# Optimization experiments

Measured on AMD Instinct MI355X. Metric: run time of the kernel, lower is better.

Reference implementation:

```python
import jax, jax.numpy as jnp
import numpy as np

B, T, D = 2, 2048, 1024
H, DH, P = 16, 64, 512


def setup_inputs() -> dict:
    key = jax.random.key(0)
    ks = jax.random.split(key, 7)
    s = 0.02
    return {
        "x": jax.random.normal(ks[0], (B, T, D), jnp.float32),
        "prefix_k": jax.random.normal(ks[1], (B, H, P, DH), jnp.float32),
        "prefix_v": jax.random.normal(ks[2], (B, H, P, DH), jnp.float32),
        "Wq": jax.random.normal(ks[3], (D, D), jnp.float32) * s,
        "Wk": jax.random.normal(ks[4], (D, D), jnp.float32) * s,
        "Wv": jax.random.normal(ks[5], (D, D), jnp.float32) * s,
        "Wo": jax.random.normal(ks[6], (D, D), jnp.float32) * s,
    }


def reference(x, prefix_k, prefix_v, Wq, Wk, Wv, Wo):
    b, t, c = x.shape
    h, dh = H, DH
    # nn.Linear without bias: y = x @ W.T
    q = (x @ Wq.T).reshape(b, t, h, dh).transpose(0, 2, 1, 3)  # [B,H,T,Dh]
    k = (x @ Wk.T).reshape(b, t, h, dh).transpose(0, 2, 1, 3)
    v = (x @ Wv.T).reshape(b, t, h, dh).transpose(0, 2, 1, 3)
    k = jnp.concatenate([prefix_k, k], axis=2)  # [B,H,P+T,Dh]
    v = jnp.concatenate([prefix_v, v], axis=2)
    scale = 1.0 / jnp.sqrt(jnp.float32(dh))
    att = jnp.einsum("bhqd,bhkd->bhqk", q, k) * scale  # [B,H,T,P+T]
    att = jax.nn.softmax(att, axis=-1)  # no causal mask in source
    y = jnp.einsum("bhqk,bhkd->bhqd", att, v)  # [B,H,T,Dh]
    y = y.transpose(0, 2, 1, 3).reshape(b, t, c)
    return y @ Wo.T
```

## Files before the change

### kernel.cpp

```cpp
#include <hip/hip_runtime.h>
#include <cstdint>

#define Bv  2
#define Tv  2048
#define Dv  1024
#define Hv  16
#define DHv 64
#define Pv  512
#define Lv  2560

typedef __attribute__((ext_vector_type(8))) short sh8;
typedef __attribute__((ext_vector_type(4))) short sh4;
typedef __attribute__((ext_vector_type(4))) float f4;
typedef __attribute__((ext_vector_type(4))) unsigned int u4v;

#define MFMA(a,b,c) __builtin_amdgcn_mfma_f32_16x16x32_bf16(a,b,c,0,0,0)

__device__ __forceinline__ unsigned short bf16_rn(float f) {
    unsigned int u = __builtin_bit_cast(unsigned int, f);
    u += 0x7FFFu + ((u >> 16) & 1u);
    return (unsigned short)(u >> 16);
}
__device__ __forceinline__ float bf16_f(unsigned short h) {
    unsigned int u = ((unsigned int)h) << 16;
    return __builtin_bit_cast(float, u);
}
__device__ __forceinline__ unsigned int fbits(float f) {
    return __builtin_bit_cast(unsigned int, f);
}

__device__ __forceinline__ void gload16(const unsigned short* g, unsigned short* l) {
    __builtin_amdgcn_global_load_lds(
        (const __attribute__((address_space(1))) unsigned int*)(g),
        (__attribute__((address_space(3))) unsigned int*)(l),
        16, 0, 0);
}

__device__ __forceinline__ sh8 packP(const f4 a, const f4 b) {
    float e0 = __builtin_amdgcn_exp2f(a[0]), e1 = __builtin_amdgcn_exp2f(a[1]);
    float e2 = __builtin_amdgcn_exp2f(a[2]), e3 = __builtin_amdgcn_exp2f(a[3]);
    float f0 = __builtin_amdgcn_exp2f(b[0]), f1 = __builtin_amdgcn_exp2f(b[1]);
    float f2 = __builtin_amdgcn_exp2f(b[2]), f3 = __builtin_amdgcn_exp2f(b[3]);
    u4v d;
    d[0] = __builtin_amdgcn_perm(fbits(e1), fbits(e0), 0x07060302u);
    d[1] = __builtin_amdgcn_perm(fbits(e3), fbits(e2), 0x07060302u);
    d[2] = __builtin_amdgcn_perm(fbits(f1), fbits(f0), 0x07060302u);
    d[3] = __builtin_amdgcn_perm(fbits(f3), fbits(f2), 0x07060302u);
    return __builtin_bit_cast(sh8, d);
}

__global__ __launch_bounds__(256) void prep_convert(
    const float* __restrict__ x,  const float* __restrict__ Wq,
    const float* __restrict__ Wk, const float* __restrict__ Wv,
    const float* __restrict__ pk, const float* __restrict__ Wo,
    unsigned short* __restrict__ xb,  unsigned short* __restrict__ wqb,
    unsigned short* __restrict__ wkb, unsigned short* __restrict__ wvb,
    unsigned short* __restrict__ pkb, unsigned short* __restrict__ woh)
{
    int i = blockIdx.x * 256 + threadIdx.x;
    const float* src; unsigned short* dst; int off;
    if      (i < 1048576) { src = x;  dst = xb;  off = i; }
    else if (i < 1310720) { src = Wq; dst = wqb; off = i - 1048576; }
    else if (i < 1572864) { src = Wk; dst = wkb; off = i - 1310720; }
    else if (i < 1835008) { src = Wv; dst = wvb; off = i - 1572864; }
    else if (i < 2097152) { src = pk; dst = pkb; off = i - 1835008; }
    else                  { src = Wo; dst = woh; off = i - 2097152; }
    float4 v = reinterpret_cast<const float4*>(src)[off];
    sh4 h;
    h[0] = (short)bf16_rn(v.x); h[1] = (short)bf16_rn(v.y);
    h[2] = (short)bf16_rn(v.z); h[3] = (short)bf16_rn(v.w);
    reinterpret_cast<sh4*>(dst)[off] = h;
}

__global__ __launch_bounds__(256) void prep_transpose(
    const float* __restrict__ pv, unsigned short* __restrict__ pvtb)
{
    __shared__ unsigned short Tls[64][66];
    const int tid = threadIdx.x;
    const int bh = blockIdx.x >> 3, pt = blockIdx.x & 7;
    #pragma unroll
    for (int i = 0; i < 4; i++) {
        int id = i * 256 + tid;
        int p = id >> 4, c4 = (id & 15) << 2;
        float4 v = *reinterpret_cast<const float4*>(
            &pv[((size_t)bh * Pv + pt * 64 + p) * DHv + c4]);
        Tls[c4+0][p] = bf16_rn(v.x);
        Tls[c4+1][p] = bf16_rn(v.y);
        Tls[c4+2][p] = bf16_rn(v.z);
        Tls[c4+3][p] = bf16_rn(v.w);
    }
    __syncthreads();
    #pragma unroll
    for (int i = 0; i < 2; i++) {
        int id = i * 256 + tid;
        int d = id >> 3, u = id & 7;
        sh4 lo, hi;
        #pragma unroll
        for (int j = 0; j < 4; j++) {
            lo[j] = (short)Tls[d][u * 8 + j];
            hi[j] = (short)Tls[d][u * 8 + 4 + j];
        }
        int p0 = ((u >> 2) & 1) * 32 + (u & 1) * 16 + ((u >> 1) & 1) * 4;
        size_t base = ((size_t)bh * DHv + d) * Pv + pt * 64;
        *reinterpret_cast<sh4*>(&pvtb[base + p0])     = lo;
        *reinterpret_cast<sh4*>(&pvtb[base + p0 + 8]) = hi;
    }
}

__global__ __launch_bounds__(256) void qkv_gemm(
    const unsigned short* __restrict__ xb,
    const unsigned short* __restrict__ wqb, const unsigned short* __restrict__ wkb,
    const unsigned short* __restrict__ wvb,
    unsigned short* __restrict__ qb, unsigned short* __restrict__ kb,
    unsigned short* __restrict__ vtb)
{
    __shared__ __align__(16) unsigned short As[128 * 64], Bs[128 * 64];
    const int tid = threadIdx.x;
    const int lane = tid & 63, w = tid >> 6;
    const int g = lane >> 4, tx = lane & 15;
    const int wr = w >> 1, wc = w & 1;
    const int m0 = blockIdx.x * 128, n0 = blockIdx.y * 128;
    const int z = blockIdx.z;
    const unsigned short* Wb = (z == 0) ? wqb : (z == 1) ? wkb : wvb;
    const int srow = lane >> 3, scol = lane & 7;

    f4 acc[4][4] = {};

    for (int k0 = 0; k0 < Dv; k0 += 64) {
        #pragma unroll
        for (int c = 0; c < 4; c++) {
            int row = w * 32 + c * 8 + srow;
            int su = (scol ^ (row & 7)) << 3;
            gload16(&xb[(size_t)(m0 + row) * Dv + k0 + su], &As[(w * 32 + c * 8) * 64]);
            gload16(&Wb[(size_t)(n0 + row) * Dv + k0 + su], &Bs[(w * 32 + c * 8) * 64]);
        }
        __syncthreads();
        #pragma unroll
        for (int ks = 0; ks < 2; ks++) {
            sh8 fa[4], fb[4];
            #pragma unroll
            for (int mi = 0; mi < 4; mi++) {
                int r = wr * 64 + mi * 16 + tx;
                fa[mi] = *reinterpret_cast<const sh8*>(&As[(r * 64 + ks * 32 + g * 8) ^ ((r & 7) << 3)]);
            }
            #pragma unroll
            for (int ni = 0; ni < 4; ni++) {
                int r = wc * 64 + ni * 16 + tx;
                fb[ni] = *reinterpret_cast<const sh8*>(&Bs[(r * 64 + ks * 32 + g * 8) ^ ((r & 7) << 3)]);
            }
            if (z < 2) {
                #pragma unroll
                for (int mi = 0; mi < 4; mi++)
                    #pragma unroll
                    for (int ni = 0; ni < 4; ni++)
                        acc[mi][ni] = MFMA(fb[ni], fa[mi], acc[mi][ni]);
            } else {
                #pragma unroll
                for (int mi = 0; mi < 4; mi++)
                    #pragma unroll
                    for (int ni = 0; ni < 4; ni++)
                        acc[mi][ni] = MFMA(fa[mi], fb[ni], acc[mi][ni]);
            }
        }
        __syncthreads();
    }

    if (z < 2) {
        unsigned short* ob = (z == 0) ? qb : kb;
        const float sc = (z == 0) ? 0.1803368801f : 1.0f;
        #pragma unroll
        for (int mi = 0; mi < 4; mi++)
            #pragma unroll
            for (int ni = 0; ni < 4; ni++) {
                int m = m0 + wr * 64 + mi * 16 + tx;
                int n = n0 + wc * 64 + ni * 16 + g * 4;
                sh4 pkd;
                #pragma unroll
                for (int i = 0; i < 4; i++) pkd[i] = (short)bf16_rn(acc[mi][ni][i] * sc);
                *reinterpret_cast<sh4*>(&ob[(size_t)m * Dv + n]) = pkd;
            }
    } else {
        const int tb0 = ((m0 + wr * 64) & (Tv - 1));
        const int b   = (m0 + wr * 64) >> 11;
        #pragma unroll
        for (int mi = 0; mi < 4; mi++)
            #pragma unroll
            for (int ni = 0; ni < 4; ni++) {
                int t = tb0 + ((mi & 2) << 4) + (g << 3) + ((mi & 1) << 2);
                int n = n0 + wc * 64 + ni * 16 + tx;
                int h = n >> 6, dh = n & 63;
                sh4 pkd;
                #pragma unroll
                for (int i = 0; i < 4; i++) pkd[i] = (short)bf16_rn(acc[mi][ni][i]);
                *reinterpret_cast<sh4*>(&vtb[(((size_t)(b * Hv + h)) * DHv + dh) * Tv + t]) = pkd;
            }
    }
}

__global__ __launch_bounds__(256) void flash_mfma(
    const unsigned short* __restrict__ qbuf, const unsigned short* __restrict__ kb,
    const unsigned short* __restrict__ vtb,
    const unsigned short* __restrict__ pkb, const unsigned short* __restrict__ pvtb,
    unsigned short* __restrict__ yh)
{
    __shared__ __align__(16) unsigned short Ks[2][64 * 64], Vs[2][64 * 64];
    __shared__ float olex[2][4][64];
    const int tid = threadIdx.x;
    const int lane = tid & 63, w = tid >> 6;
    const int kw = w & 1, qw = w >> 1;
    const int g = lane >> 4, tx = lane & 15;
    const int pblk = blockIdx.x;
    const int L = (pblk & 7) * 64 + (pblk >> 3);
    const int qt = L & 15;
    const int bh = L >> 4;
    const int b = bh >> 4, h = bh & 15;
    const int srow = lane >> 3, scol = lane & 7;

    sh8 qf[4][2];
    #pragma unroll
    for (int qg = 0; qg < 4; qg++) {
        size_t base = ((size_t)(b * Tv) + qt * 128 + qw * 64 + qg * 16 + tx) * Dv + h * 64;
        qf[qg][0] = *reinterpret_cast<const sh8*>(&qbuf[base + g * 8]);
        qf[qg][1] = *reinterpret_cast<const sh8*>(&qbuf[base + 32 + g * 8]);
    }

    f4 o[4][4] = {};
    f4 ol[4] = {};
    sh8 onesf;
    #pragma unroll
    for (int j = 0; j < 8; j++) onesf[j] = (short)0x3F80;

    const int r0 = w * 16 + srow, r1 = r0 + 8;
    const int su0 = (scol ^ (r0 & 7)) << 3;
    const int su1 = (scol ^ (r1 & 7)) << 3;
    const unsigned short* ka0 = &pkb[((size_t)bh * Pv + r0) * DHv + su0];
    const unsigned short* ka1 = &pkb[((size_t)bh * Pv + r1) * DHv + su1];
    const unsigned short* va0 = &pvtb[((size_t)bh * DHv + r0) * Pv + su0];
    const unsigned short* va1 = &pvtb[((size_t)bh * DHv + r1) * Pv + su1];

    auto stage = [&](int buf) {
        gload16(ka0, &Ks[buf][(w * 16    ) * 64]);
        gload16(ka1, &Ks[buf][(w * 16 + 8) * 64]);
        gload16(va0, &Vs[buf][(w * 16    ) * 64]);
        gload16(va1, &Vs[buf][(w * 16 + 8) * 64]);
    };
    auto advance = [&](int nt) {
        if (nt == 7) {
            ka0 = &kb[((size_t)(b * Tv) + r0) * Dv + h * 64 + su0];
            ka1 = &kb[((size_t)(b * Tv) + r1) * Dv + h * 64 + su1];
            va0 = &vtb[((size_t)bh * DHv + r0) * Tv + su0];
            va1 = &vtb[((size_t)bh * DHv + r1) * Tv + su1];
        } else if (nt < 7) { ka0 += 64 * DHv; ka1 += 64 * DHv; va0 += 64; va1 += 64; }
        else               { ka0 += 64 * Dv;  ka1 += 64 * Dv;  va0 += 64; va1 += 64; }
    };

    auto compute = [&](int cur) {
        sh8 kf[2][2], vf[4];
        #pragma unroll
        for (int nf = 0; nf < 2; nf++) {
            int rk = 32 * kw + nf * 16 + tx;
            kf[nf][0] = *reinterpret_cast<const sh8*>(
                &Ks[cur][(rk * 64 + g * 8) ^ ((rk & 7) << 3)]);
            kf[nf][1] = *reinterpret_cast<const sh8*>(
                &Ks[cur][(rk * 64 + 32 + g * 8) ^ ((rk & 7) << 3)]);
        }
        #pragma unroll
        for (int nf = 0; nf < 4; nf++) {
            int rv = nf * 16 + tx;
            vf[nf] = *reinterpret_cast<const sh8*>(
                &Vs[cur][(rv * 64 + 32 * kw + g * 8) ^ ((rv & 7) << 3)]);
        }
        #pragma unroll
        for (int qg = 0; qg < 4; qg++) {
            f4 sa = {}, sb = {};
            sa = MFMA(kf[0][0], qf[qg][0], sa); sa = MFMA(kf[0][1], qf[qg][1], sa);
            sb = MFMA(kf[1][0], qf[qg][0], sb); sb = MFMA(kf[1][1], qf[qg][1], sb);
            sh8 pf = packP(sa, sb);
            #pragma unroll
            for (int nf = 0; nf < 4; nf++)
                o[qg][nf] = MFMA(vf[nf], pf, o[qg][nf]);
            ol[qg] = MFMA(onesf, pf, ol[qg]);
        }
    };

    stage(0); advance(0);
    asm volatile("s_waitcnt vmcnt(0)" ::: "memory");
    __builtin_amdgcn_s_barrier();
    __builtin_amdgcn_sched_barrier(0);
    int cur = 0;

    for (int t = 0; t < Lv / 64 - 1; t++) {
        stage(cur ^ 1); advance(t + 1);
        asm volatile("s_waitcnt vmcnt(4)" ::: "memory");
        __builtin_amdgcn_s_barrier();
        __builtin_amdgcn_sched_barrier(0);
        compute(cur);
        __builtin_amdgcn_sched_barrier(0);
        __builtin_amdgcn_s_barrier();
        cur ^= 1;
    }
    asm volatile("s_waitcnt vmcnt(0)" ::: "memory");
    __builtin_amdgcn_s_barrier();
    __builtin_amdgcn_sched_barrier(0);
    compute(cur);

    float* ex = qw ? reinterpret_cast<float*>(Vs) : reinterpret_cast<float*>(Ks);
    if (kw) {
        #pragma unroll
        for (int qg = 0; qg < 4; qg++) {
            #pragma unroll
            for (int nf = 0; nf < 4; nf++)
                *reinterpret_cast<f4*>(&ex[((qg * 4 + nf) * 64 + lane) * 4]) = o[qg][nf];
            olex[qw][qg][lane] = ol[qg][0];
        }
    }
    __syncthreads();
    if (!kw) {
        #pragma unroll
        for (int qg = 0; qg < 4; qg++) {
            float l = ol[qg][0] + olex[qw][qg][lane];
            float inv = 1.0f / l;
            size_t ybase = ((size_t)(b * Tv) + qt * 128 + qw * 64 + qg * 16 + tx) * Dv + h * 64;
            #pragma unroll
            for (int nf = 0; nf < 4; nf++) {
                f4 op = o[qg][nf] +
                    *reinterpret_cast<const f4*>(&ex[((qg * 4 + nf) * 64 + lane) * 4]);
                sh4 ph;
                #pragma unroll
                for (int i = 0; i < 4; i++) ph[i] = (short)bf16_rn(op[i] * inv);
                *reinterpret_cast<sh4*>(&yh[ybase + nf * 16 + g * 4]) = ph;
            }
        }
    }
}

__global__ __launch_bounds__(256) void out_gemm(
    const unsigned short* __restrict__ yh,
    const unsigned short* __restrict__ woh,
    float* __restrict__ out)
{
    __shared__ __align__(16) unsigned short As[64 * 64], Bs[128 * 64];
    const int tid = threadIdx.x;
    const int lane = tid & 63, w = tid >> 6;
    const int g = lane >> 4, tx = lane & 15;
    const int wr = w >> 1, wc = w & 1;
    const int m0 = blockIdx.x * 64, n0 = blockIdx.y * 128;
    const int srow = lane >> 3, scol = lane & 7;

    f4 acc[2][4] = {};

    for (int k0 = 0; k0 < Dv; k0 += 64) {
        #pragma unroll
        for (int c = 0; c < 2; c++) {
            int row = w * 16 + c * 8 + srow;
            int su = (scol ^ (row & 7)) << 3;
            gload16(&yh[(size_t)(m0 + row) * Dv + k0 + su], &As[(w * 16 + c * 8) * 64]);
        }
        #pragma unroll
        for (int c = 0; c < 4; c++) {
            int row = w * 32 + c * 8 + srow;
            int su = (scol ^ (row & 7)) << 3;
            gload16(&woh[(size_t)(n0 + row) * Dv + k0 + su], &Bs[(w * 32 + c * 8) * 64]);
        }
        __syncthreads();
        #pragma unroll
        for (int ks = 0; ks < 2; ks++) {
            sh8 fa[2], fb[4];
            #pragma unroll
            for (int mi = 0; mi < 2; mi++) {
                int r = wr * 32 + mi * 16 + tx;
                fa[mi] = *reinterpret_cast<const sh8*>(&As[(r * 64 + ks * 32 + g * 8) ^ ((r & 7) << 3)]);
            }
            #pragma unroll
            for (int ni = 0; ni < 4; ni++) {
                int r = wc * 64 + ni * 16 + tx;
                fb[ni] = *reinterpret_cast<const sh8*>(&Bs[(r * 64 + ks * 32 + g * 8) ^ ((r & 7) << 3)]);
            }
            #pragma unroll
            for (int mi = 0; mi < 2; mi++)
                #pragma unroll
                for (int ni = 0; ni < 4; ni++)
                    acc[mi][ni] = MFMA(fb[ni], fa[mi], acc[mi][ni]);
        }
        __syncthreads();
    }

    #pragma unroll
    for (int mi = 0; mi < 2; mi++)
        #pragma unroll
        for (int ni = 0; ni < 4; ni++) {
            int m = m0 + wr * 32 + mi * 16 + tx;
            int n = n0 + wc * 64 + ni * 16 + g * 4;
            *reinterpret_cast<float4*>(&out[(size_t)m * Dv + n]) =
                make_float4(acc[mi][ni][0], acc[mi][ni][1], acc[mi][ni][2], acc[mi][ni][3]);
        }
}

extern "C" void kernel_launch(void* const* d_in, const int* in_sizes, int n_in,
                              void* d_out, int out_size, void* d_ws, size_t ws_size,
                              hipStream_t stream)
{
    const float* x  = (const float*)d_in[0];
    const float* pk = (const float*)d_in[1];
    const float* pv = (const float*)d_in[2];
    const float* Wq = (const float*)d_in[3];
    const float* Wk = (const float*)d_in[4];
    const float* Wv = (const float*)d_in[5];
    const float* Wo = (const float*)d_in[6];

    const size_t M1 = 1048576;
    unsigned short* ws  = (unsigned short*)d_ws;
    unsigned short* xb   = ws;
    unsigned short* wqb  = ws + 4  * M1;
    unsigned short* wkb  = ws + 5  * M1;
    unsigned short* wvb  = ws + 6  * M1;
    unsigned short* woh  = ws + 7  * M1;
    unsigned short* pkb  = ws + 8  * M1;
    unsigned short* pvtb = ws + 9  * M1;
    unsigned short* qb   = ws + 10 * M1;
    unsigned short* kb   = ws + 14 * M1;
    unsigned short* vtb  = ws + 18 * M1;
    unsigned short* yh   = ws + 22 * M1;

    prep_convert<<<9216, 256, 0, stream>>>(x, Wq, Wk, Wv, pk, Wo,
                                           xb, wqb, wkb, wvb, pkb, woh);
    prep_transpose<<<256, 256, 0, stream>>>(pv, pvtb);
    qkv_gemm<<<dim3(32, 8, 3), 256, 0, stream>>>(xb, wqb, wkb, wvb, qb, kb, vtb);
    flash_mfma<<<dim3(Bv * Hv * (Tv / 128)), 256, 0, stream>>>(qb, kb, vtb, pkb, pvtb, yh);
    out_gemm<<<dim3(64, 8), 256, 0, stream>>>(yh, woh, (float*)d_out);
}
```

Baseline: 121.0 us.

## Triple-buffer K/V tiles in flash kernel and merge prep kernels

The flash attention loop moves from double to triple buffering of K/V tiles in LDS. Each iteration now waits on one barrier before issuing the next stage's loads, where the old loop used two barriers, so global loads can run two tiles ahead of compute. The two preprocessing kernels (bf16 convert and prefix-V transpose) are merged into one launch to cut launch overhead. LDS use for K/V grows by half, which may reduce occupancy. Dropping the trailing barrier relies on the three-buffer rotation to prevent overwriting a tile still being read.

Result: no change. 120.9 us (-0.1%).

```diff
diff --git a/kernel.cpp b/kernel.cpp
--- a/kernel.cpp
+++ b/kernel.cpp
@@ -8,6 +8,7 @@
 #define DHv 64
 #define Pv  512
 #define Lv  2560
+#define NT  (Lv / 64)
 
 typedef __attribute__((ext_vector_type(8))) short sh8;
 typedef __attribute__((ext_vector_type(4))) short sh4;
@@ -49,61 +50,63 @@
     return __builtin_bit_cast(sh8, d);
 }
 
-__global__ __launch_bounds__(256) void prep_convert(
+__global__ __launch_bounds__(256) void prep_all(
     const float* __restrict__ x,  const float* __restrict__ Wq,
     const float* __restrict__ Wk, const float* __restrict__ Wv,
     const float* __restrict__ pk, const float* __restrict__ Wo,
+    const float* __restrict__ pv,
     unsigned short* __restrict__ xb,  unsigned short* __restrict__ wqb,
     unsigned short* __restrict__ wkb, unsigned short* __restrict__ wvb,
-    unsigned short* __restrict__ pkb, unsigned short* __restrict__ woh)
-{
-    int i = blockIdx.x * 256 + threadIdx.x;
-    const float* src; unsigned short* dst; int off;
-    if      (i < 1048576) { src = x;  dst = xb;  off = i; }
-    else if (i < 1310720) { src = Wq; dst = wqb; off = i - 1048576; }
-    else if (i < 1572864) { src = Wk; dst = wkb; off = i - 1310720; }
-    else if (i < 1835008) { src = Wv; dst = wvb; off = i - 1572864; }
-    else if (i < 2097152) { src = pk; dst = pkb; off = i - 1835008; }
-    else                  { src = Wo; dst = woh; off = i - 2097152; }
-    float4 v = reinterpret_cast<const float4*>(src)[off];
-    sh4 h;
-    h[0] = (short)bf16_rn(v.x); h[1] = (short)bf16_rn(v.y);
-    h[2] = (short)bf16_rn(v.z); h[3] = (short)bf16_rn(v.w);
-    reinterpret_cast<sh4*>(dst)[off] = h;
-}
-
-__global__ __launch_bounds__(256) void prep_transpose(
-    const float* __restrict__ pv, unsigned short* __restrict__ pvtb)
+    unsigned short* __restrict__ pkb, unsigned short* __restrict__ woh,
+    unsigned short* __restrict__ pvtb)
 {
     __shared__ unsigned short Tls[64][66];
+    const int blk = blockIdx.x;
     const int tid = threadIdx.x;
-    const int bh = blockIdx.x >> 3, pt = blockIdx.x & 7;
-    #pragma unroll
-    for (int i = 0; i < 4; i++) {
-        int id = i * 256 + tid;
-        int p = id >> 4, c4 = (id & 15) << 2;
-        float4 v = *reinterpret_cast<const float4*>(
-            &pv[((size_t)bh * Pv + pt * 64 + p) * DHv + c4]);
-        Tls[c4+0][p] = bf16_rn(v.x);
-        Tls[c4+1][p] = bf16_rn(v.y);
-        Tls[c4+2][p] = bf16_rn(v.z);
-        Tls[c4+3][p] = bf16_rn(v.w);
-    }
-    __syncthreads();
-    #pragma unroll
-    for (int i = 0; i < 2; i++) {
-        int id = i * 256 + tid;
-        int d = id >> 3, u = id & 7;
-        sh4 lo, hi;
-        #pragma unroll
-        for (int j = 0; j < 4; j++) {
-            lo[j] = (short)Tls[d][u * 8 + j];
-            hi[j] = (short)Tls[d][u * 8 + 4 + j];
-        }
-        int p0 = ((u >> 2) & 1) * 32 + (u & 1) * 16 + ((u >> 1) & 1) * 4;
-        size_t base = ((size_t)bh * DHv + d) * Pv + pt * 64;
-        *reinterpret_cast<sh4*>(&pvtb[base + p0])     = lo;
-        *reinterpret_cast<sh4*>(&pvtb[base + p0 + 8]) = hi;
+    if (blk < 9216) {
+        int i = blk * 256 + tid;
+        const float* src; unsigned short* dst; int off;
+        if      (i < 1048576) { src = x;  dst = xb;  off = i; }
+        else if (i < 1310720) { src = Wq; dst = wqb; off = i - 1048576; }
+        else if (i < 1572864) { src = Wk; dst = wkb; off = i - 1310720; }
+        else if (i < 1835008) { src = Wv; dst = wvb; off = i - 1572864; }
+        else if (i < 2097152) { src = pk; dst = pkb; off = i - 1835008; }
+        else                  { src = Wo; dst = woh; off = i - 2097152; }
+        float4 v = reinterpret_cast<const float4*>(src)[off];
+        sh4 h;
+        h[0] = (short)bf16_rn(v.x); h[1] = (short)bf16_rn(v.y);
+        h[2] = (short)bf16_rn(v.z); h[3] = (short)bf16_rn(v.w);
+        reinterpret_cast<sh4*>(dst)[off] = h;
+    } else {
+        const int bb = blk - 9216;
+        const int bh = bb >> 3, pt = bb & 7;
+        #pragma unroll
+        for (int i = 0; i < 4; i++) {
+            int id = i * 256 + tid;
+            int p = id >> 4, c4 = (id & 15) << 2;
+            float4 v = *reinterpret_cast<const float4*>(
+                &pv[((size_t)bh * Pv + pt * 64 + p) * DHv + c4]);
+            Tls[c4+0][p] = bf16_rn(v.x);
+            Tls[c4+1][p] = bf16_rn(v.y);
+            Tls[c4+2][p] = bf16_rn(v.z);
+            Tls[c4+3][p] = bf16_rn(v.w);
+        }
+        __syncthreads();
+        #pragma unroll
+        for (int i = 0; i < 2; i++) {
+            int id = i * 256 + tid;
+            int d = id >> 3, u = id & 7;
+            sh4 lo, hi;
+            #pragma unroll
+            for (int j = 0; j < 4; j++) {
+                lo[j] = (short)Tls[d][u * 8 + j];
+                hi[j] = (short)Tls[d][u * 8 + 4 + j];
+            }
+            int p0 = ((u >> 2) & 1) * 32 + (u & 1) * 16 + ((u >> 1) & 1) * 4;
+            size_t base = ((size_t)bh * DHv + d) * Pv + pt * 64;
+            *reinterpret_cast<sh4*>(&pvtb[base + p0])     = lo;
+            *reinterpret_cast<sh4*>(&pvtb[base + p0 + 8]) = hi;
+        }
     }
 }
 
@@ -203,7 +206,7 @@
     const unsigned short* __restrict__ pkb, const unsigned short* __restrict__ pvtb,
     unsigned short* __restrict__ yh)
 {
-    __shared__ __align__(16) unsigned short Ks[2][64 * 64], Vs[2][64 * 64];
+    __shared__ __align__(16) unsigned short Ks[3][64 * 64], Vs[3][64 * 64];
     __shared__ float olex[2][4][64];
     const int tid = threadIdx.x;
     const int lane = tid & 63, w = tid >> 6;
@@ -284,21 +287,26 @@
     };
 
     stage(0); advance(0);
-    asm volatile("s_waitcnt vmcnt(0)" ::: "memory");
-    __builtin_amdgcn_s_barrier();
-    __builtin_amdgcn_sched_barrier(0);
-    int cur = 0;
-
-    for (int t = 0; t < Lv / 64 - 1; t++) {
-        stage(cur ^ 1); advance(t + 1);
+    stage(1); advance(1);
+    int cur = 0, stg = 2;
+
+    #pragma unroll 1
+    for (int t = 0; t < NT - 2; t++) {
         asm volatile("s_waitcnt vmcnt(4)" ::: "memory");
         __builtin_amdgcn_s_barrier();
         __builtin_amdgcn_sched_barrier(0);
+        stage(stg); advance(t + 2);
         compute(cur);
         __builtin_amdgcn_sched_barrier(0);
-        __builtin_amdgcn_s_barrier();
-        cur ^= 1;
-    }
+        cur = (cur == 2) ? 0 : cur + 1;
+        stg = (stg == 2) ? 0 : stg + 1;
+    }
+    asm volatile("s_waitcnt vmcnt(4)" ::: "memory");
+    __builtin_amdgcn_s_barrier();
+    __builtin_amdgcn_sched_barrier(0);
+    compute(cur);
+    __builtin_amdgcn_sched_barrier(0);
+    cur = (cur == 2) ? 0 : cur + 1;
     asm volatile("s_waitcnt vmcnt(0)" ::: "memory");
     __builtin_amdgcn_s_barrier();
     __builtin_amdgcn_sched_barrier(0);
@@ -422,9 +430,8 @@
     unsigned short* vtb  = ws + 18 * M1;
     unsigned short* yh   = ws + 22 * M1;
 
-    prep_convert<<<9216, 256, 0, stream>>>(x, Wq, Wk, Wv, pk, Wo,
-                                           xb, wqb, wkb, wvb, pkb, woh);
-    prep_transpose<<<256, 256, 0, stream>>>(pv, pvtb);
+    prep_all<<<9472, 256, 0, stream>>>(x, Wq, Wk, Wv, pk, Wo, pv,
+                                       xb, wqb, wkb, wvb, pkb, woh, pvtb);
     qkv_gemm<<<dim3(32, 8, 3), 256, 0, stream>>>(xb, wqb, wkb, wvb, qb, kb, vtb);
     flash_mfma<<<dim3(Bv * Hv * (Tv / 128)), 256, 0, stream>>>(qb, kb, vtb, pkb, pvtb, yh);
     out_gemm<<<dim3(64, 8), 256, 0, stream>>>(yh, woh, (float*)d_out);
```
